# Kernel tuning notes

Measured on AMD Instinct MI355X. Metric: run time of the kernel, lower is better.

## Reference

```python
import jax, jax.numpy as jnp
import numpy as np

N_NODES = 50000
N_EDGES = 800000
IN_CH = 128
HID = 64
N_LAYERS = 14
EPS_MSG = 1e-7
EPS_SM = 1e-16
LN_EPS = 1e-5


def setup_inputs() -> dict:
    key = jax.random.key(0)
    ks = jax.random.split(key, 8)
    x = jax.random.normal(ks[0], (N_NODES, IN_CH), dtype=jnp.float32)
    edge_index = jax.random.randint(ks[1], (2, N_EDGES), 0, N_NODES, dtype=jnp.int64)
    enc_W = jax.random.normal(ks[2], (IN_CH, HID), dtype=jnp.float32) / np.sqrt(IN_CH)
    enc_b = jnp.zeros((HID,), dtype=jnp.float32)
    mlp_W = jax.random.normal(ks[3], (N_LAYERS, HID, HID), dtype=jnp.float32) / np.sqrt(HID)
    mlp_b = jnp.zeros((N_LAYERS, HID), dtype=jnp.float32)
    t = jnp.ones((N_LAYERS,), dtype=jnp.float32)  # learn_t, init t=1.0
    return {"x": x, "edge_index": edge_index, "enc_W": enc_W, "enc_b": enc_b,
            "mlp_W": mlp_W, "mlp_b": mlp_b, "t": t}


def _layernorm(h):
    # LayerNorm(elementwise_affine=False) over last dim
    mu = jnp.mean(h, axis=-1, keepdims=True)
    var = jnp.mean((h - mu) ** 2, axis=-1, keepdims=True)
    return (h - mu) * jax.lax.rsqrt(var + LN_EPS)


def _segment_softmax(scores, seg, num_segments):
    # per-target-node, per-channel softmax over incoming edges
    m = jax.ops.segment_max(scores, seg, num_segments=num_segments)
    e = jnp.exp(scores - m[seg])
    s = jax.ops.segment_sum(e, seg, num_segments=num_segments)
    return e / (s[seg] + EPS_SM)


def _genconv(h, src, dst, W, b, t):
    # GENConv: msg = relu(x_j) + eps; softmax_sg aggregation (weights detached);
    # out = MLP(aggr + x) where MLP is a single Linear
    msg = jax.nn.relu(h[src]) + EPS_MSG                       # [E, H]
    alpha = _segment_softmax(t * msg, dst, N_NODES)           # [E, H]
    alpha = jax.lax.stop_gradient(alpha)                      # 'softmax_sg'
    aggr = jax.ops.segment_sum(msg * alpha, dst, num_segments=N_NODES)
    return (aggr + h) @ W + b


def reference(x, edge_index, enc_W, enc_b, mlp_W, mlp_b, t):
    src, dst = edge_index[0], edge_index[1]
    h = x @ enc_W + enc_b                                     # node encoder
    h = _genconv(h, src, dst, mlp_W[0], mlp_b[0], t[0])       # layers[0].conv

    def body(carry, params):
        W, b, tt = params
        y = jax.nn.relu(_layernorm(carry))                    # res+ pre-norm/act
        y = _genconv(y, src, dst, W, b, tt)                   # dropout inactive (eval)
        return carry + y, None

    h, _ = jax.lax.scan(body, h, (mlp_W[1:], mlp_b[1:], t[1:]))
    h = jax.nn.relu(_layernorm(h))                            # final norm + act
    return jax.nn.log_softmax(h, axis=-1)
```

## Files before the change

kernel.cpp:

```cpp
#include <hip/hip_runtime.h>

#define NN 50000
#define NE 800000
#define INC 128
#define HIDC 64
#define NL 14
#define EPS_MSG 1e-7f
#define EPS_SM 1e-16f
#define LN_EPS 1e-5f

#define SCAN_B 256
#define NB_SCAN ((NN + SCAN_B - 1) / SCAN_B)

__device__ __forceinline__ float wave_sum(float v) {
    #pragma unroll
    for (int o = 32; o > 0; o >>= 1) v += __shfl_xor(v, o, 64);
    return v;
}
__device__ __forceinline__ float wave_max(float v) {
    #pragma unroll
    for (int o = 32; o > 0; o >>= 1) v = fmaxf(v, __shfl_xor(v, o, 64));
    return v;
}
__device__ __forceinline__ float bcast(float x, int l) {
    return __int_as_float(__builtin_amdgcn_readlane(__float_as_int(x), l));
}
__device__ __forceinline__ unsigned pack_bf2(float lo, float hi) {
    unsigned ul = __float_as_uint(lo); ul += 0x7fffu + ((ul >> 16) & 1u);
    unsigned uh = __float_as_uint(hi); uh += 0x7fffu + ((uh >> 16) & 1u);
    return (ul >> 16) | (uh & 0xffff0000u);
}

__global__ void k_hist(const int* __restrict__ dst, int* __restrict__ deg) {
    int i = blockIdx.x * blockDim.x + threadIdx.x;
    if (i < NE) atomicAdd(&deg[dst[i]], 1);
}

__global__ void k_part(const int* __restrict__ deg, int* __restrict__ part) {
    __shared__ int sm[SCAN_B];
    int b = blockIdx.x;
    int i = b * SCAN_B + threadIdx.x;
    sm[threadIdx.x] = (i < NN) ? deg[i] : 0;
    __syncthreads();
    for (int s = SCAN_B / 2; s > 0; s >>= 1) {
        if (threadIdx.x < s) sm[threadIdx.x] += sm[threadIdx.x + s];
        __syncthreads();
    }
    if (threadIdx.x == 0) part[b] = sm[0];
}

__global__ void k_scanpart(const int* __restrict__ part, int* __restrict__ partOfs) {
    __shared__ int sm[SCAN_B];
    int t = threadIdx.x;
    int own = (t < NB_SCAN) ? part[t] : 0;
    sm[t] = own;
    __syncthreads();
    for (int o = 1; o < SCAN_B; o <<= 1) {
        int v = (t >= o) ? sm[t - o] : 0;
        __syncthreads();
        sm[t] += v;
        __syncthreads();
    }
    if (t < NB_SCAN) partOfs[t] = sm[t] - own;
}

__global__ void k_scanfinal(const int* __restrict__ deg, const int* __restrict__ partOfs,
                            int* __restrict__ rowOfs) {
    __shared__ int sm[SCAN_B];
    int b = blockIdx.x, t = threadIdx.x;
    int i = b * SCAN_B + t;
    int d = (i < NN) ? deg[i] : 0;
    sm[t] = d;
    __syncthreads();
    for (int o = 1; o < SCAN_B; o <<= 1) {
        int v = (t >= o) ? sm[t - o] : 0;
        __syncthreads();
        sm[t] += v;
        __syncthreads();
    }
    if (i < NN) rowOfs[i] = partOfs[b] + sm[t] - d;
    if (i == 0) rowOfs[NN] = NE;
}

__global__ void k_scatter(const int* __restrict__ src, const int* __restrict__ dst,
                          const int* __restrict__ rowOfs, int* __restrict__ cur,
                          int* __restrict__ csr) {
    int i = blockIdx.x * blockDim.x + threadIdx.x;
    if (i < NE) {
        int d = dst[i];
        int p = rowOfs[d] + atomicAdd(&cur[d], 1);
        csr[p] = src[i];
    }
}

__global__ __launch_bounds__(256) void k_enc(const float* __restrict__ x,
                                             const float* __restrict__ W,
                                             const float* __restrict__ bias,
                                             float* __restrict__ h,
                                             unsigned* __restrict__ B0) {
    __shared__ float XL[32 * INC];
    __shared__ float WL[INC * HIDC];
    int tid = threadIdx.x;
    for (int i = tid; i < (INC * HIDC) / 4; i += 256)
        ((float4*)WL)[i] = ((const float4*)W)[i];
    int r0 = blockIdx.x * 32;
    for (int i = tid; i < (32 * INC) / 4; i += 256) {
        int row = i >> 5;
        float4 val = make_float4(0.f, 0.f, 0.f, 0.f);
        if (r0 + row < NN) val = ((const float4*)x)[(size_t)(r0 + row) * 32 + (i & 31)];
        ((float4*)XL)[i] = val;
    }
    __syncthreads();
    int lane = tid & 63, w = tid >> 6;
    float bv = bias[lane];
    #pragma unroll
    for (int i = 0; i < 4; i++) {
        int ra = w * 8 + i * 2, rb = ra + 1;
        float a0 = 0.f, a1 = 0.f, a2 = 0.f, a3 = 0.f;
        float c0 = 0.f, c1 = 0.f, c2 = 0.f, c3 = 0.f;
        #pragma unroll
        for (int k = 0; k < INC; k += 4) {
            float4 xa = *(const float4*)&XL[ra * INC + k];
            float4 xb = *(const float4*)&XL[rb * INC + k];
            float w0 = WL[(k + 0) * HIDC + lane];
            float w1 = WL[(k + 1) * HIDC + lane];
            float w2 = WL[(k + 2) * HIDC + lane];
            float w3 = WL[(k + 3) * HIDC + lane];
            a0 = fmaf(xa.x, w0, a0); a1 = fmaf(xa.y, w1, a1);
            a2 = fmaf(xa.z, w2, a2); a3 = fmaf(xa.w, w3, a3);
            c0 = fmaf(xb.x, w0, c0); c1 = fmaf(xb.y, w1, c1);
            c2 = fmaf(xb.z, w2, c2); c3 = fmaf(xb.w, w3, c3);
        }
        int ga = r0 + ra, gb = r0 + rb;
        float va = bv + ((a0 + a1) + (a2 + a3));
        float vb = bv + ((c0 + c1) + (c2 + c3));
        float pa = __shfl_xor(va, 1, 64);
        float pb = __shfl_xor(vb, 1, 64);
        if (ga < NN) {
            h[(size_t)ga * HIDC + lane] = va;
            if (!(lane & 1)) B0[(size_t)ga * 32 + (lane >> 1)] = pack_bf2(va, pa);
        }
        if (gb < NN) {
            h[(size_t)gb * HIDC + lane] = vb;
            if (!(lane & 1)) B0[(size_t)gb * 32 + (lane >> 1)] = pack_bf2(vb, pb);
        }
    }
}

template<bool FIRST>
__global__ __launch_bounds__(256) void k_aggr(const float* __restrict__ henc,
                                              const unsigned* __restrict__ Bin,
                                              const int* __restrict__ rowOfs,
                                              const int* __restrict__ csr,
                                              const float* __restrict__ tptr,
                                              float* __restrict__ A) {
    int lane = threadIdx.x & 63;
    int v = (blockIdx.x * 256 + threadIdx.x) >> 6;
    int g = lane >> 4;
    int c = lane & 15;
    float tl = (*tptr) * 1.44269504088896f;

    int e0 = rowOfs[v], e1 = rowOfs[v + 1];
    float se0 = 0.f, se1 = 0.f, se2 = 0.f, se3 = 0.f;
    float sw0 = 0.f, sw1 = 0.f, sw2 = 0.f, sw3 = 0.f;
    for (int e = e0; e < e1; e += 16) {
        #pragma unroll
        for (int j = 0; j < 4; j++) {
            int ee = e + 4 * j + g;
            bool valid = ee < e1;
            int s = csr[valid ? ee : e0];
            uint2 q = ((const uint2*)Bin)[(size_t)s * 16 + c];
            float g0 = __uint_as_float(q.x << 16);
            float g1 = __uint_as_float(q.x & 0xffff0000u);
            float g2 = __uint_as_float(q.y << 16);
            float g3 = __uint_as_float(q.y & 0xffff0000u);
            g0 = fmaxf(g0, 0.f) + EPS_MSG;
            g1 = fmaxf(g1, 0.f) + EPS_MSG;
            g2 = fmaxf(g2, 0.f) + EPS_MSG;
            g3 = fmaxf(g3, 0.f) + EPS_MSG;
            float w0 = valid ? exp2f(tl * g0) : 0.f;
            float w1 = valid ? exp2f(tl * g1) : 0.f;
            float w2 = valid ? exp2f(tl * g2) : 0.f;
            float w3 = valid ? exp2f(tl * g3) : 0.f;
            se0 += w0; sw0 = fmaf(g0, w0, sw0);
            se1 += w1; sw1 = fmaf(g1, w1, sw1);
            se2 += w2; sw2 = fmaf(g2, w2, sw2);
            se3 += w3; sw3 = fmaf(g3, w3, sw3);
        }
    }
    #pragma unroll
    for (int m = 16; m <= 32; m <<= 1) {
        se0 += __shfl_xor(se0, m, 64); sw0 += __shfl_xor(sw0, m, 64);
        se1 += __shfl_xor(se1, m, 64); sw1 += __shfl_xor(sw1, m, 64);
        se2 += __shfl_xor(se2, m, 64); sw2 += __shfl_xor(sw2, m, 64);
        se3 += __shfl_xor(se3, m, 64); sw3 += __shfl_xor(sw3, m, 64);
    }
    if (g == 0) {
        float4 r;
        r.x = sw0 / (se0 + EPS_SM);
        r.y = sw1 / (se1 + EPS_SM);
        r.z = sw2 / (se2 + EPS_SM);
        r.w = sw3 / (se3 + EPS_SM);
        if (FIRST) {
            float4 s4 = ((const float4*)henc)[(size_t)v * 16 + c];
            r.x += s4.x; r.y += s4.y; r.z += s4.z; r.w += s4.w;
        }
        ((float4*)A)[(size_t)v * 16 + c] = r;
    }
}

template<bool LNRES, int MODE>
__global__ __launch_bounds__(256) void k_mlp(const float* __restrict__ A,
                                             float* __restrict__ h,
                                             unsigned* __restrict__ Bout,
                                             const float* __restrict__ W,
                                             const float* __restrict__ b) {
    __shared__ float WL[HIDC * HIDC];
    for (int i = threadIdx.x; i < (HIDC * HIDC) / 4; i += 256)
        ((float4*)WL)[i] = ((const float4*)W)[i];
    __syncthreads();

    int lane = threadIdx.x & 63;
    int wid = (blockIdx.x * 256 + threadIdx.x) >> 6;
    int nw = (gridDim.x * 256) >> 6;
    float bv = b[lane];

    for (int v = wid; v < NN; v += nw) {
        float a = A[(size_t)v * HIDC + lane];
        float base = bv;
        if (LNRES) {
            float hv = h[(size_t)v * HIDC + lane];
            float mu = wave_sum(hv) * (1.f / 64.f);
            float d = hv - mu;
            float var = wave_sum(d * d) * (1.f / 64.f);
            a += fmaxf(d * rsqrtf(var + LN_EPS), 0.f);
            base += hv;
        }
        float a0 = 0.f, a1 = 0.f, a2 = 0.f, a3 = 0.f;
        #pragma unroll
        for (int k = 0; k < 64; k += 4) {
            a0 = fmaf(bcast(a, k + 0), WL[(k + 0) * HIDC + lane], a0);
            a1 = fmaf(bcast(a, k + 1), WL[(k + 1) * HIDC + lane], a1);
            a2 = fmaf(bcast(a, k + 2), WL[(k + 2) * HIDC + lane], a2);
            a3 = fmaf(bcast(a, k + 3), WL[(k + 3) * HIDC + lane], a3);
        }
        float acc = base + ((a0 + a1) + (a2 + a3));

        if (MODE == 1) {
            float mu = wave_sum(acc) * (1.f / 64.f);
            float d = acc - mu;
            float var = wave_sum(d * d) * (1.f / 64.f);
            float z = fmaxf(d * rsqrtf(var + LN_EPS), 0.f);
            float m = wave_max(z);
            float s2 = wave_sum(exp2f((z - m) * 1.44269504088896f));
            h[(size_t)v * HIDC + lane] = z - (m + __logf(s2));
        } else {
            h[(size_t)v * HIDC + lane] = acc;
            float mu = wave_sum(acc) * (1.f / 64.f);
            float d = acc - mu;
            float var = wave_sum(d * d) * (1.f / 64.f);
            float y = fmaxf(d * rsqrtf(var + LN_EPS), 0.f);
            float yp = __shfl_xor(y, 1, 64);
            if (!(lane & 1)) Bout[(size_t)v * 32 + (lane >> 1)] = pack_bf2(y, yp);
        }
    }
}

extern "C" void kernel_launch(void* const* d_in, const int* in_sizes, int n_in,
                              void* d_out, int out_size, void* d_ws, size_t ws_size,
                              hipStream_t stream) {
    const float* x    = (const float*)d_in[0];
    const int*   ei   = (const int*)d_in[1];
    const float* encW = (const float*)d_in[2];
    const float* encb = (const float*)d_in[3];
    const float* mlpW = (const float*)d_in[4];
    const float* mlpb = (const float*)d_in[5];
    const float* t    = (const float*)d_in[6];

    float* h = (float*)d_out;

    char* ws = (char*)d_ws;
    size_t off = 0;
    auto alloc = [&](size_t bytes) -> void* {
        void* p = ws + off;
        off += (bytes + 255) / 256 * 256;
        return p;
    };
    float*    henc   = (float*)alloc((size_t)NN * HIDC * 4);
    float*    A      = (float*)alloc((size_t)NN * HIDC * 4);
    unsigned* B0     = (unsigned*)alloc((size_t)NN * 32 * 4);
    unsigned* B1     = (unsigned*)alloc((size_t)NN * 32 * 4);
    int*      deg    = (int*)alloc((size_t)NN * 4);
    int*      cur    = (int*)alloc((size_t)NN * 4);
    int*      rowOfs = (int*)alloc((size_t)(NN + 1) * 4);
    int*      part   = (int*)alloc((size_t)NB_SCAN * 4);
    int*      partOf = (int*)alloc((size_t)NB_SCAN * 4);
    int*      csr    = (int*)alloc((size_t)NE * 4);

    const int* src = ei;
    const int* dst = ei + NE;

    hipMemsetAsync(deg, 0, (size_t)NN * 4, stream);
    hipMemsetAsync(cur, 0, (size_t)NN * 4, stream);

    k_hist<<<(NE + 255) / 256, 256, 0, stream>>>(dst, deg);
    k_part<<<NB_SCAN, SCAN_B, 0, stream>>>(deg, part);
    k_scanpart<<<1, SCAN_B, 0, stream>>>(part, partOf);
    k_scanfinal<<<NB_SCAN, SCAN_B, 0, stream>>>(deg, partOf, rowOfs);
    k_scatter<<<(NE + 255) / 256, 256, 0, stream>>>(src, dst, rowOfs, cur, csr);

    k_enc<<<(NN + 31) / 32, 256, 0, stream>>>(x, encW, encb, henc, B0);

    k_aggr<true><<<12500, 256, 0, stream>>>(henc, B0, rowOfs, csr, t, A);
    k_mlp<false, 0><<<2048, 256, 0, stream>>>(A, h, B1, mlpW, mlpb);

    for (int l = 1; l < NL - 1; l++) {
        unsigned* Bi = (l & 1) ? B1 : B0;
        unsigned* Bo = (l & 1) ? B0 : B1;
        k_aggr<false><<<12500, 256, 0, stream>>>(nullptr, Bi, rowOfs, csr, t + l, A);
        k_mlp<true, 0><<<2048, 256, 0, stream>>>(A, h, Bo,
                                                 mlpW + (size_t)l * HIDC * HIDC,
                                                 mlpb + (size_t)l * HIDC);
    }
    k_aggr<false><<<12500, 256, 0, stream>>>(nullptr, B1, rowOfs, csr, t + (NL - 1), A);
    k_mlp<true, 1><<<2048, 256, 0, stream>>>(A, h, nullptr,
                                             mlpW + (size_t)(NL - 1) * HIDC * HIDC,
                                             mlpb + (size_t)(NL - 1) * HIDC);
}
```

Measured before the change: 1.089 ms.

## Prescale bf16 messages by t*log2e upstream and simplify aggregation inner loop

The producer kernels now store relu(h)*t*log2(e) in the bf16 message buffers, so the aggregation loop drops the relu, epsilon add and multiply and calls raw v_exp_f32. The epsilon and 1/(t*log2e) rescale are applied once per node after the softmax-weighted sum. The CSR array now stores byte offsets (src<<7), which removes the index multiply, and full 16-edge chunks run without validity masks. The scatter uses a copied rowOfs as its cursor. Moving the epsilon outside the exponent, dropping it from the softmax weights, and skipping the overflow handling of exp2f slightly change numerics.

Result: faster. 1.030 ms (-5.4%).

```diff
diff --git a/kernel.cpp b/kernel.cpp
--- a/kernel.cpp
+++ b/kernel.cpp
@@ -8,6 +8,7 @@
 #define EPS_MSG 1e-7f
 #define EPS_SM 1e-16f
 #define LN_EPS 1e-5f
+#define LOG2E 1.44269504088896f
 
 #define SCAN_B 256
 #define NB_SCAN ((NN + SCAN_B - 1) / SCAN_B)
@@ -24,6 +25,9 @@
 }
 __device__ __forceinline__ float bcast(float x, int l) {
     return __int_as_float(__builtin_amdgcn_readlane(__float_as_int(x), l));
+}
+__device__ __forceinline__ float fexp2(float x) {
+    float r; asm("v_exp_f32 %0, %1" : "=v"(r) : "v"(x)); return r;
 }
 __device__ __forceinline__ unsigned pack_bf2(float lo, float hi) {
     unsigned ul = __float_as_uint(lo); ul += 0x7fffu + ((ul >> 16) & 1u);
@@ -83,19 +87,18 @@
 }
 
 __global__ void k_scatter(const int* __restrict__ src, const int* __restrict__ dst,
-                          const int* __restrict__ rowOfs, int* __restrict__ cur,
-                          int* __restrict__ csr) {
+                          int* __restrict__ rowCur, int* __restrict__ csrB) {
     int i = blockIdx.x * blockDim.x + threadIdx.x;
     if (i < NE) {
-        int d = dst[i];
-        int p = rowOfs[d] + atomicAdd(&cur[d], 1);
-        csr[p] = src[i];
+        int p = atomicAdd(&rowCur[dst[i]], 1);
+        csrB[p] = src[i] << 7;
     }
 }
 
 __global__ __launch_bounds__(256) void k_enc(const float* __restrict__ x,
                                              const float* __restrict__ W,
                                              const float* __restrict__ bias,
+                                             const float* __restrict__ tptr,
                                              float* __restrict__ h,
                                              unsigned* __restrict__ B0) {
     __shared__ float XL[32 * INC];
@@ -113,6 +116,7 @@
     __syncthreads();
     int lane = tid & 63, w = tid >> 6;
     float bv = bias[lane];
+    float sc = tptr[0] * LOG2E;
     #pragma unroll
     for (int i = 0; i < 4; i++) {
         int ra = w * 8 + i * 2, rb = ra + 1;
@@ -134,15 +138,16 @@
         int ga = r0 + ra, gb = r0 + rb;
         float va = bv + ((a0 + a1) + (a2 + a3));
         float vb = bv + ((c0 + c1) + (c2 + c3));
-        float pa = __shfl_xor(va, 1, 64);
-        float pb = __shfl_xor(vb, 1, 64);
+        float sa = sc * fmaxf(va, 0.f), sb = sc * fmaxf(vb, 0.f);
+        float pa = __shfl_xor(sa, 1, 64);
+        float pb = __shfl_xor(sb, 1, 64);
         if (ga < NN) {
             h[(size_t)ga * HIDC + lane] = va;
-            if (!(lane & 1)) B0[(size_t)ga * 32 + (lane >> 1)] = pack_bf2(va, pa);
+            if (!(lane & 1)) B0[(size_t)ga * 32 + (lane >> 1)] = pack_bf2(sa, pa);
         }
         if (gb < NN) {
             h[(size_t)gb * HIDC + lane] = vb;
-            if (!(lane & 1)) B0[(size_t)gb * 32 + (lane >> 1)] = pack_bf2(vb, pb);
+            if (!(lane & 1)) B0[(size_t)gb * 32 + (lane >> 1)] = pack_bf2(sb, pb);
         }
     }
 }
@@ -151,37 +156,51 @@
 __global__ __launch_bounds__(256) void k_aggr(const float* __restrict__ henc,
                                               const unsigned* __restrict__ Bin,
                                               const int* __restrict__ rowOfs,
-                                              const int* __restrict__ csr,
+                                              const int* __restrict__ csrB,
                                               const float* __restrict__ tptr,
                                               float* __restrict__ A) {
     int lane = threadIdx.x & 63;
     int v = (blockIdx.x * 256 + threadIdx.x) >> 6;
     int g = lane >> 4;
     int c = lane & 15;
-    float tl = (*tptr) * 1.44269504088896f;
+    const char* basec = (const char*)Bin + (c << 3);
+    float invs = 1.0f / (tptr[0] * LOG2E);
 
     int e0 = rowOfs[v], e1 = rowOfs[v + 1];
     float se0 = 0.f, se1 = 0.f, se2 = 0.f, se3 = 0.f;
     float sw0 = 0.f, sw1 = 0.f, sw2 = 0.f, sw3 = 0.f;
-    for (int e = e0; e < e1; e += 16) {
+    int e = e0;
+    for (; e + 16 <= e1; e += 16) {
+        #pragma unroll
+        for (int j = 0; j < 4; j++) {
+            int off = csrB[e + 4 * j + g];
+            uint2 q = *(const uint2*)(basec + off);
+            float g0 = __uint_as_float(q.x << 16);
+            float g1 = __uint_as_float(q.x & 0xffff0000u);
+            float g2 = __uint_as_float(q.y << 16);
+            float g3 = __uint_as_float(q.y & 0xffff0000u);
+            float w0 = fexp2(g0), w1 = fexp2(g1), w2 = fexp2(g2), w3 = fexp2(g3);
+            se0 += w0; sw0 = fmaf(g0, w0, sw0);
+            se1 += w1; sw1 = fmaf(g1, w1, sw1);
+            se2 += w2; sw2 = fmaf(g2, w2, sw2);
+            se3 += w3; sw3 = fmaf(g3, w3, sw3);
+        }
+    }
+    if (e < e1) {
         #pragma unroll
         for (int j = 0; j < 4; j++) {
             int ee = e + 4 * j + g;
             bool valid = ee < e1;
-            int s = csr[valid ? ee : e0];
-            uint2 q = ((const uint2*)Bin)[(size_t)s * 16 + c];
+            int off = csrB[valid ? ee : e0];
+            uint2 q = *(const uint2*)(basec + off);
             float g0 = __uint_as_float(q.x << 16);
             float g1 = __uint_as_float(q.x & 0xffff0000u);
             float g2 = __uint_as_float(q.y << 16);
             float g3 = __uint_as_float(q.y & 0xffff0000u);
-            g0 = fmaxf(g0, 0.f) + EPS_MSG;
-            g1 = fmaxf(g1, 0.f) + EPS_MSG;
-            g2 = fmaxf(g2, 0.f) + EPS_MSG;
-            g3 = fmaxf(g3, 0.f) + EPS_MSG;
-            float w0 = valid ? exp2f(tl * g0) : 0.f;
-            float w1 = valid ? exp2f(tl * g1) : 0.f;
-            float w2 = valid ? exp2f(tl * g2) : 0.f;
-            float w3 = valid ? exp2f(tl * g3) : 0.f;
+            float w0 = valid ? fexp2(g0) : 0.f;
+            float w1 = valid ? fexp2(g1) : 0.f;
+            float w2 = valid ? fexp2(g2) : 0.f;
+            float w3 = valid ? fexp2(g3) : 0.f;
             se0 += w0; sw0 = fmaf(g0, w0, sw0);
             se1 += w1; sw1 = fmaf(g1, w1, sw1);
             se2 += w2; sw2 = fmaf(g2, w2, sw2);
@@ -197,10 +216,10 @@
     }
     if (g == 0) {
         float4 r;
-        r.x = sw0 / (se0 + EPS_SM);
-        r.y = sw1 / (se1 + EPS_SM);
-        r.z = sw2 / (se2 + EPS_SM);
-        r.w = sw3 / (se3 + EPS_SM);
+        r.x = sw0 / (se0 + EPS_SM) * invs + EPS_MSG;
+        r.y = sw1 / (se1 + EPS_SM) * invs + EPS_MSG;
+        r.z = sw2 / (se2 + EPS_SM) * invs + EPS_MSG;
+        r.w = sw3 / (se3 + EPS_SM) * invs + EPS_MSG;
         if (FIRST) {
             float4 s4 = ((const float4*)henc)[(size_t)v * 16 + c];
             r.x += s4.x; r.y += s4.y; r.z += s4.z; r.w += s4.w;
@@ -214,7 +233,8 @@
                                              float* __restrict__ h,
                                              unsigned* __restrict__ Bout,
                                              const float* __restrict__ W,
-                                             const float* __restrict__ b) {
+                                             const float* __restrict__ b,
+                                             const float* __restrict__ tnext) {
     __shared__ float WL[HIDC * HIDC];
     for (int i = threadIdx.x; i < (HIDC * HIDC) / 4; i += 256)
         ((float4*)WL)[i] = ((const float4*)W)[i];
@@ -224,6 +244,7 @@
     int wid = (blockIdx.x * 256 + threadIdx.x) >> 6;
     int nw = (gridDim.x * 256) >> 6;
     float bv = b[lane];
+    float sc = (MODE == 0) ? tnext[0] * LOG2E : 0.f;
 
     for (int v = wid; v < NN; v += nw) {
         float a = A[(size_t)v * HIDC + lane];
@@ -252,14 +273,14 @@
             float var = wave_sum(d * d) * (1.f / 64.f);
             float z = fmaxf(d * rsqrtf(var + LN_EPS), 0.f);
             float m = wave_max(z);
-            float s2 = wave_sum(exp2f((z - m) * 1.44269504088896f));
+            float s2 = wave_sum(fexp2((z - m) * LOG2E));
             h[(size_t)v * HIDC + lane] = z - (m + __logf(s2));
         } else {
             h[(size_t)v * HIDC + lane] = acc;
             float mu = wave_sum(acc) * (1.f / 64.f);
             float d = acc - mu;
             float var = wave_sum(d * d) * (1.f / 64.f);
-            float y = fmaxf(d * rsqrtf(var + LN_EPS), 0.f);
+            float y = sc * fmaxf(d * rsqrtf(var + LN_EPS), 0.f);
             float yp = __shfl_xor(y, 1, 64);
             if (!(lane & 1)) Bout[(size_t)v * 32 + (lane >> 1)] = pack_bf2(y, yp);
         }
@@ -291,39 +312,39 @@
     unsigned* B0     = (unsigned*)alloc((size_t)NN * 32 * 4);
     unsigned* B1     = (unsigned*)alloc((size_t)NN * 32 * 4);
     int*      deg    = (int*)alloc((size_t)NN * 4);
-    int*      cur    = (int*)alloc((size_t)NN * 4);
     int*      rowOfs = (int*)alloc((size_t)(NN + 1) * 4);
+    int*      rowCur = (int*)alloc((size_t)NN * 4);
     int*      part   = (int*)alloc((size_t)NB_SCAN * 4);
     int*      partOf = (int*)alloc((size_t)NB_SCAN * 4);
-    int*      csr    = (int*)alloc((size_t)NE * 4);
+    int*      csrB   = (int*)alloc((size_t)NE * 4);
 
     const int* src = ei;
     const int* dst = ei + NE;
 
     hipMemsetAsync(deg, 0, (size_t)NN * 4, stream);
-    hipMemsetAsync(cur, 0, (size_t)NN * 4, stream);
 
     k_hist<<<(NE + 255) / 256, 256, 0, stream>>>(dst, deg);
     k_part<<<NB_SCAN, SCAN_B, 0, stream>>>(deg, part);
     k_scanpart<<<1, SCAN_B, 0, stream>>>(part, partOf);
     k_scanfinal<<<NB_SCAN, SCAN_B, 0, stream>>>(deg, partOf, rowOfs);
-    k_scatter<<<(NE + 255) / 256, 256, 0, stream>>>(src, dst, rowOfs, cur, csr);
-
-    k_enc<<<(NN + 31) / 32, 256, 0, stream>>>(x, encW, encb, henc, B0);
-
-    k_aggr<true><<<12500, 256, 0, stream>>>(henc, B0, rowOfs, csr, t, A);
-    k_mlp<false, 0><<<2048, 256, 0, stream>>>(A, h, B1, mlpW, mlpb);
+    hipMemcpyAsync(rowCur, rowOfs, (size_t)NN * 4, hipMemcpyDeviceToDevice, stream);
+    k_scatter<<<(NE + 255) / 256, 256, 0, stream>>>(src, dst, rowCur, csrB);
+
+    k_enc<<<(NN + 31) / 32, 256, 0, stream>>>(x, encW, encb, t, henc, B0);
+
+    k_aggr<true><<<12500, 256, 0, stream>>>(henc, B0, rowOfs, csrB, t, A);
+    k_mlp<false, 0><<<2048, 256, 0, stream>>>(A, h, B1, mlpW, mlpb, t + 1);
 
     for (int l = 1; l < NL - 1; l++) {
         unsigned* Bi = (l & 1) ? B1 : B0;
         unsigned* Bo = (l & 1) ? B0 : B1;
-        k_aggr<false><<<12500, 256, 0, stream>>>(nullptr, Bi, rowOfs, csr, t + l, A);
+        k_aggr<false><<<12500, 256, 0, stream>>>(nullptr, Bi, rowOfs, csrB, t + l, A);
         k_mlp<true, 0><<<2048, 256, 0, stream>>>(A, h, Bo,
                                                  mlpW + (size_t)l * HIDC * HIDC,
-                                                 mlpb + (size_t)l * HIDC);
-    }
-    k_aggr<false><<<12500, 256, 0, stream>>>(nullptr, B1, rowOfs, csr, t + (NL - 1), A);
+                                                 mlpb + (size_t)l * HIDC, t + l + 1);
+    }
+    k_aggr<false><<<12500, 256, 0, stream>>>(nullptr, B1, rowOfs, csrB, t + (NL - 1), A);
     k_mlp<true, 1><<<2048, 256, 0, stream>>>(A, h, nullptr,
                                              mlpW + (size_t)(NL - 1) * HIDC * HIDC,
-                                             mlpb + (size_t)(NL - 1) * HIDC);
-}
+                                             mlpb + (size_t)(NL - 1) * HIDC, nullptr);
+}
```
